# Kernel tuning notes

Measured on AMD Instinct MI355X. Metric: run time of the kernel, lower is better.

## Reference

```python
import jax, jax.numpy as jnp
import numpy as np

N, C, H, W = 128, 3, 256, 256
MAXNORM = 5.371920351148152
MAX_SQ = 16  # static bound for data-dependent squaring loop
PADE_B = [6.476475253248e+16, 3.238237626624e+16, 7771770303897600.0,
          1187353796428800.0, 129060195264000.0, 10559470521600.0,
          670442572800.0, 33522128640.0, 1323241920.0, 40840800.0,
          960960.0, 16380.0, 182.0, 1.0]


def pade13(A):
    b = PADE_B
    I = jnp.eye(A.shape[-1], dtype=A.dtype)
    A2 = A @ A
    A4 = A2 @ A2
    A6 = A4 @ A2
    U = A @ (A6 @ (b[13] * A6 + b[11] * A4 + b[9] * A2)
             + b[7] * A6 + b[5] * A4 + b[3] * A2 + b[1] * I)
    V = (A6 @ (b[12] * A6 + b[10] * A4 + b[8] * A2)
         + b[6] * A6 + b[4] * A4 + b[2] * A2 + b[0] * I)
    return U, V


def expm_affine(theta):  # theta: [N,2,3] -> exp of padded 3x3, top 2 rows
    n = theta.shape[0]
    A = jnp.concatenate([theta, jnp.zeros((n, 1, 3), theta.dtype)], axis=1)
    fro = jnp.sqrt(jnp.sum(A * A, axis=(1, 2), keepdims=True))
    n_sq = jnp.maximum(0.0, jnp.ceil(jnp.log2(fro / MAXNORM)))
    Asc = A / (2.0 ** n_sq)
    U, V = pade13(Asc)
    R = jnp.linalg.solve(U + V, -U + V)
    k = n_sq.reshape(n).astype(jnp.int32)
    def body(i, Rc):
        return jnp.where((i < k)[:, None, None], jnp.matmul(Rc, Rc), Rc)
    R = jax.lax.fori_loop(0, MAX_SQ, body, R)
    return R[:, :2, :]


def affine_grid(theta, Ho, Wo):  # align_corners=True
    xs = jnp.linspace(-1.0, 1.0, Wo, dtype=theta.dtype)
    ys = jnp.linspace(-1.0, 1.0, Ho, dtype=theta.dtype)
    gy, gx = jnp.meshgrid(ys, xs, indexing='ij')          # [Ho,Wo]
    base = jnp.stack([gx, gy, jnp.ones_like(gx)], axis=-1)  # [Ho,Wo,3]
    return jnp.einsum('hwk,nck->nhwc', base, theta)        # [N,Ho,Wo,2]


def grid_sample(x, grid):  # bilinear, zeros padding, align_corners=True
    _, _, Hi, Wi = x.shape
    ix = (grid[..., 0] + 1.0) * 0.5 * (Wi - 1)
    iy = (grid[..., 1] + 1.0) * 0.5 * (Hi - 1)
    ix0 = jnp.floor(ix)
    iy0 = jnp.floor(iy)
    ix1 = ix0 + 1.0
    iy1 = iy0 + 1.0
    wx1 = ix - ix0; wx0 = 1.0 - wx1
    wy1 = iy - iy0; wy0 = 1.0 - wy1

    def gather(yy, xx):
        valid = ((yy >= 0) & (yy < Hi) & (xx >= 0) & (xx < Wi))
        yc = jnp.clip(yy, 0, Hi - 1).astype(jnp.int32)
        xc = jnp.clip(xx, 0, Wi - 1).astype(jnp.int32)
        vals = jax.vmap(lambda img, y, xi: img[:, y, xi])(x, yc, xc)  # [N,C,Ho,Wo]
        return vals * valid[:, None].astype(x.dtype)

    return (gather(iy0, ix0) * (wy0 * wx0)[:, None]
            + gather(iy0, ix1) * (wy0 * wx1)[:, None]
            + gather(iy1, ix0) * (wy1 * wx0)[:, None]
            + gather(iy1, ix1) * (wy1 * wx1)[:, None])


def setup_inputs() -> dict:
    key = jax.random.key(0)
    k1, k2 = jax.random.split(key)
    x = jax.random.normal(k1, (N, C, H, W), dtype=jnp.float32)
    theta = 0.1 * jax.random.normal(k2, (N, 6), dtype=jnp.float32)
    return {"x": x, "theta": theta}


def reference(x, theta):
    th = expm_affine(theta.reshape(-1, 2, 3))  # [N,2,3]
    grid = affine_grid(th, H, W)               # [N,H,W,2]
    return grid_sample(x, grid)                # [N,C,H,W]
```

## Files before the change

### kernel.cpp

```cpp
#include <hip/hip_runtime.h>

#define Ndim 128
#define Cdim 3
#define Hdim 256
#define Wdim 256
#define HW (Hdim * Wdim)
#define MAXNORM_F 5.371920351148152f

typedef float vf2 __attribute__((ext_vector_type(2)));
typedef float vf4 __attribute__((ext_vector_type(4)));

__device__ __forceinline__ void mm3f(const float a[3][3], const float b[3][3], float c[3][3]) {
    #pragma unroll
    for (int i = 0; i < 3; ++i)
        #pragma unroll
        for (int j = 0; j < 3; ++j) {
            float s = 0.0f;
            #pragma unroll
            for (int k = 0; k < 3; ++k) s = fmaf(a[i][k], b[k][j], s);
            c[i][j] = s;
        }
}

__global__ void expm_kernel(const float* __restrict__ theta, float* __restrict__ thOut) {
    int n = blockIdx.x * blockDim.x + threadIdx.x;
    if (n >= Ndim) return;

    const float b[14] = {6.476475253248e+16f, 3.238237626624e+16f, 7771770303897600.0f,
                         1187353796428800.0f, 129060195264000.0f, 10559470521600.0f,
                         670442572800.0f, 33522128640.0f, 1323241920.0f, 40840800.0f,
                         960960.0f, 16380.0f, 182.0f, 1.0f};

    float A[3][3];
    #pragma unroll
    for (int j = 0; j < 3; ++j) {
        A[0][j] = theta[n * 6 + j];
        A[1][j] = theta[n * 6 + 3 + j];
        A[2][j] = 0.0f;
    }

    float fro2 = 0.0f;
    #pragma unroll
    for (int i = 0; i < 3; ++i)
        #pragma unroll
        for (int j = 0; j < 3; ++j) fro2 = fmaf(A[i][j], A[i][j], fro2);
    float fro = sqrtf(fro2);

    float nsq = fmaxf(0.0f, ceilf(log2f(fro / MAXNORM_F)));
    int k = (int)nsq;
    float sc = exp2f(-nsq);
    #pragma unroll
    for (int i = 0; i < 3; ++i)
        #pragma unroll
        for (int j = 0; j < 3; ++j) A[i][j] *= sc;

    float A2[3][3], A4[3][3], A6[3][3], P[3][3], Wm[3][3], T[3][3], U[3][3], V[3][3];
    mm3f(A, A, A2);
    mm3f(A2, A2, A4);
    mm3f(A4, A2, A6);

    #pragma unroll
    for (int i = 0; i < 3; ++i)
        #pragma unroll
        for (int j = 0; j < 3; ++j)
            P[i][j] = b[13] * A6[i][j] + b[11] * A4[i][j] + b[9] * A2[i][j];
    mm3f(A6, P, T);
    #pragma unroll
    for (int i = 0; i < 3; ++i)
        #pragma unroll
        for (int j = 0; j < 3; ++j)
            Wm[i][j] = T[i][j] + b[7] * A6[i][j] + b[5] * A4[i][j] + b[3] * A2[i][j]
                       + (i == j ? b[1] : 0.0f);
    mm3f(A, Wm, U);

    #pragma unroll
    for (int i = 0; i < 3; ++i)
        #pragma unroll
        for (int j = 0; j < 3; ++j)
            P[i][j] = b[12] * A6[i][j] + b[10] * A4[i][j] + b[8] * A2[i][j];
    mm3f(A6, P, T);
    #pragma unroll
    for (int i = 0; i < 3; ++i)
        #pragma unroll
        for (int j = 0; j < 3; ++j)
            V[i][j] = T[i][j] + b[6] * A6[i][j] + b[4] * A4[i][j] + b[2] * A2[i][j]
                      + (i == j ? b[0] : 0.0f);

    float M[3][6];
    #pragma unroll
    for (int i = 0; i < 3; ++i)
        #pragma unroll
        for (int j = 0; j < 3; ++j) {
            M[i][j]     = U[i][j] + V[i][j];
            M[i][j + 3] = V[i][j] - U[i][j];
        }
    #pragma unroll
    for (int col = 0; col < 3; ++col) {
        int piv = col;
        float best = fabsf(M[col][col]);
        for (int r = col + 1; r < 3; ++r) {
            float v = fabsf(M[r][col]);
            if (v > best) { best = v; piv = r; }
        }
        if (piv != col) {
            #pragma unroll
            for (int j = 0; j < 6; ++j) {
                float t = M[col][j]; M[col][j] = M[piv][j]; M[piv][j] = t;
            }
        }
        float inv = 1.0f / M[col][col];
        #pragma unroll
        for (int j = 0; j < 6; ++j) M[col][j] *= inv;
        #pragma unroll
        for (int r = 0; r < 3; ++r) {
            if (r == col) continue;
            float f = M[r][col];
            #pragma unroll
            for (int j = 0; j < 6; ++j) M[r][j] -= f * M[col][j];
        }
    }
    float R[3][3];
    #pragma unroll
    for (int i = 0; i < 3; ++i)
        #pragma unroll
        for (int j = 0; j < 3; ++j) R[i][j] = M[i][j + 3];

    for (int i = 0; i < 16; ++i) {
        if (i < k) {
            float Rn[3][3];
            mm3f(R, R, Rn);
            #pragma unroll
            for (int a = 0; a < 3; ++a)
                #pragma unroll
                for (int c = 0; c < 3; ++c) R[a][c] = Rn[a][c];
        }
    }

    #pragma unroll
    for (int j = 0; j < 3; ++j) {
        thOut[n * 6 + j]     = (float)R[0][j];
        thOut[n * 6 + 3 + j] = (float)R[1][j];
    }
}

__global__ __launch_bounds__(256) void sample_kernel(const float* __restrict__ x,
                                                     const float* __restrict__ th,
                                                     float* __restrict__ out) {
    const int nwg_per_xcd = 8192 / 8;
    int bid = blockIdx.x;
    int wgid = (bid & 7) * nwg_per_xcd + (bid >> 3);

    int tw  = wgid & 3;
    int thp = (wgid >> 2) & 15;
    int n   = wgid >> 6;

    int tid = threadIdx.x;
    int wp  = tid & 31;
    int hp  = tid >> 5;
    int w0  = (tw << 6) + (wp << 1);
    int h0  = (thp << 4) + (hp << 1);

    const float* t = th + n * 6;
    float t0 = t[0], t1 = t[1], t2 = t[2], t3 = t[3], t4 = t[4], t5 = t[5];

    float Cx = 127.5f * (t2 - t0 - t1 + 1.0f);
    float Cy = 127.5f * (t5 - t3 - t4 + 1.0f);

    float ix00 = fmaf((float)w0, t0, fmaf((float)h0, t1, Cx));
    float iy00 = fmaf((float)w0, t3, fmaf((float)h0, t4, Cy));
    float ix[2][2] = {{ix00, ix00 + t0}, {ix00 + t1, ix00 + t0 + t1}};
    float iy[2][2] = {{iy00, iy00 + t3}, {iy00 + t4, iy00 + t3 + t4}};

    size_t nbase = (size_t)n * Cdim * HW;
    bool fast = (fabsf(t0) + fabsf(t1) < 2.0f) && (fabsf(t3) + fabsf(t4) < 2.0f);

    if (fast) {
        float Xminf = fminf(fminf(ix[0][0], ix[0][1]), fminf(ix[1][0], ix[1][1]));
        float Yminf = fminf(fminf(iy[0][0], iy[0][1]), fminf(iy[1][0], iy[1][1]));
        int Xmin = (int)floorf(Xminf);
        int Ymin = (int)floorf(Yminf);
        int bx = min(max(Xmin, 0), Wdim - 4);

        float wxv[2][2][4], wyv[2][2][4];
        #pragma unroll
        for (int p = 0; p < 2; ++p)
            #pragma unroll
            for (int q = 0; q < 2; ++q) {
                float fx = floorf(ix[p][q]);
                float fy = floorf(iy[p][q]);
                int ixi = (int)fx, iyi = (int)fy;
                float wx1 = ix[p][q] - fx, wx0 = 1.0f - wx1;
                float wy1 = iy[p][q] - fy, wy0 = 1.0f - wy1;
                float mx0 = ((unsigned)ixi       < (unsigned)Wdim) ? 1.0f : 0.0f;
                float mx1 = ((unsigned)(ixi + 1) < (unsigned)Wdim) ? 1.0f : 0.0f;
                float my0 = ((unsigned)iyi       < (unsigned)Hdim) ? 1.0f : 0.0f;
                float my1 = ((unsigned)(iyi + 1) < (unsigned)Hdim) ? 1.0f : 0.0f;
                float wxm0 = wx0 * mx0, wxm1 = wx1 * mx1;
                float wym0 = wy0 * my0, wym1 = wy1 * my1;

                int cxa = min(max(ixi, 0), Wdim - 1) - bx;
                int cxb = min(max(ixi + 1, 0), Wdim - 1) - bx;
                int rya = iyi - Ymin;
                #pragma unroll
                for (int j = 0; j < 4; ++j) {
                    wxv[p][q][j] = (j == cxa ? wxm0 : 0.0f) + (j == cxb ? wxm1 : 0.0f);
                    wyv[p][q][j] = (j == rya ? wym0 : 0.0f) + (j == rya + 1 ? wym1 : 0.0f);
                }
            }

        int roff[4];
        #pragma unroll
        for (int i = 0; i < 4; ++i) {
            int r = min(max(Ymin + i, 0), Hdim - 1);
            roff[i] = (r << 8) + bx;
        }

        const float* img0 = x + nbase;
        const float* img1 = img0 + HW;
        const float* img2 = img1 + HW;
        vf4 R0[4], R1[4], R2[4];
        #pragma unroll
        for (int i = 0; i < 4; ++i) __builtin_memcpy(&R0[i], img0 + roff[i], 16);
        #pragma unroll
        for (int i = 0; i < 4; ++i) __builtin_memcpy(&R1[i], img1 + roff[i], 16);
        #pragma unroll
        for (int i = 0; i < 4; ++i) __builtin_memcpy(&R2[i], img2 + roff[i], 16);

        size_t p0 = (size_t)h0 * Wdim + w0;
        size_t p1 = p0 + Wdim;

        #pragma unroll
        for (int c = 0; c < Cdim; ++c) {
            const vf4* Rw = (c == 0) ? R0 : (c == 1) ? R1 : R2;
            float res[2][2];
            #pragma unroll
            for (int p = 0; p < 2; ++p)
                #pragma unroll
                for (int q = 0; q < 2; ++q) {
                    float s = 0.0f;
                    #pragma unroll
                    for (int i = 0; i < 4; ++i) {
                        vf4 rv = Rw[i];
                        float d = fmaf(rv.x, wxv[p][q][0],
                                  fmaf(rv.y, wxv[p][q][1],
                                  fmaf(rv.z, wxv[p][q][2],
                                       rv.w * wxv[p][q][3])));
                        s = fmaf(wyv[p][q][i], d, s);
                    }
                    res[p][q] = s;
                }
            vf2 r0 = {res[0][0], res[0][1]};
            vf2 r1 = {res[1][0], res[1][1]};
            __builtin_nontemporal_store(r0, (vf2*)(out + nbase + (size_t)c * HW + p0));
            __builtin_nontemporal_store(r1, (vf2*)(out + nbase + (size_t)c * HW + p1));
        }
    } else {
        const float* img0 = x + nbase;
        #pragma unroll
        for (int p = 0; p < 2; ++p)
            #pragma unroll
            for (int q = 0; q < 2; ++q) {
                float fx = floorf(ix[p][q]);
                float fy = floorf(iy[p][q]);
                int ix0 = (int)fx, iy0 = (int)fy;
                float wx1 = ix[p][q] - fx, wx0 = 1.0f - wx1;
                float wy1 = iy[p][q] - fy, wy0 = 1.0f - wy1;
                float mx0 = ((unsigned)ix0       < (unsigned)Wdim) ? 1.0f : 0.0f;
                float mx1 = ((unsigned)(ix0 + 1) < (unsigned)Wdim) ? 1.0f : 0.0f;
                float my0 = ((unsigned)iy0       < (unsigned)Hdim) ? 1.0f : 0.0f;
                float my1 = ((unsigned)(iy0 + 1) < (unsigned)Hdim) ? 1.0f : 0.0f;
                int xc0 = min(max(ix0, 0), Wdim - 1);
                int xc1 = min(max(ix0 + 1, 0), Wdim - 1);
                int yc0 = min(max(iy0, 0), Hdim - 1);
                int yc1 = min(max(iy0 + 1, 0), Hdim - 1);
                float w00 = wy0 * wx0 * my0 * mx0;
                float w01 = wy0 * wx1 * my0 * mx1;
                float w10 = wy1 * wx0 * my1 * mx0;
                float w11 = wy1 * wx1 * my1 * mx1;
                int o00 = yc0 * Wdim + xc0, o01 = yc0 * Wdim + xc1;
                int o10 = yc1 * Wdim + xc0, o11 = yc1 * Wdim + xc1;
                #pragma unroll
                for (int c = 0; c < Cdim; ++c) {
                    const float* img = img0 + (size_t)c * HW;
                    float r = fmaf(img[o00], w00, fmaf(img[o01], w01,
                              fmaf(img[o10], w10, img[o11] * w11)));
                    out[nbase + (size_t)c * HW + (size_t)(h0 + p) * Wdim + (w0 + q)] = r;
                }
            }
    }
}

extern "C" void kernel_launch(void* const* d_in, const int* in_sizes, int n_in,
                              void* d_out, int out_size, void* d_ws, size_t ws_size,
                              hipStream_t stream) {
    const float* x     = (const float*)d_in[0];
    const float* theta = (const float*)d_in[1];
    float* out = (float*)d_out;
    float* th  = (float*)d_ws;

    expm_kernel<<<1, 128, 0, stream>>>(theta, th);

    int nblocks = Ndim * 16 * 4;
    sample_kernel<<<nblocks, 256, 0, stream>>>(x, th, out);
}
```

Baseline: 42.27 us.

## Stage bounding-box source patch in LDS via global_load_lds with square tiles

Each workgroup now covers a 32x32 output tile instead of 16x64. It computes the bounding box of the source pixels that tile needs and loads that patch for all three channels into shared memory with direct global-to-LDS loads. Each thread then does its bilinear taps from LDS instead of issuing per-thread 4x4 vector global loads, which cuts redundant global and L2 traffic. The cost is a barrier and about 40KB of LDS per workgroup, which may lower occupancy. Tiles whose patch exceeds the LDS buffer fall back to the direct-gather path.

```diff
diff --git a/kernel.cpp b/kernel.cpp
--- a/kernel.cpp
+++ b/kernel.cpp
@@ -8,7 +8,7 @@
 #define MAXNORM_F 5.371920351148152f
 
 typedef float vf2 __attribute__((ext_vector_type(2)));
-typedef float vf4 __attribute__((ext_vector_type(4)));
+typedef unsigned int uint32;
 
 __device__ __forceinline__ void mm3f(const float a[3][3], const float b[3][3], float c[3][3]) {
     #pragma unroll
@@ -146,19 +146,20 @@
 __global__ __launch_bounds__(256) void sample_kernel(const float* __restrict__ x,
                                                      const float* __restrict__ th,
                                                      float* __restrict__ out) {
+    __shared__ float lds[10240];
+
     const int nwg_per_xcd = 8192 / 8;
     int bid = blockIdx.x;
     int wgid = (bid & 7) * nwg_per_xcd + (bid >> 3);
 
-    int tw  = wgid & 3;
-    int thp = (wgid >> 2) & 15;
+    int tw  = wgid & 7;
+    int thp = (wgid >> 3) & 7;
     int n   = wgid >> 6;
 
     int tid = threadIdx.x;
-    int wp  = tid & 31;
-    int hp  = tid >> 5;
-    int w0  = (tw << 6) + (wp << 1);
-    int h0  = (thp << 4) + (hp << 1);
+    int wp = tid & 15, hp = tid >> 4;
+    int w0 = (tw << 5) + (wp << 1);
+    int h0 = (thp << 5) + (hp << 1);
 
     const float* t = th + n * 6;
     float t0 = t[0], t1 = t[1], t2 = t[2], t3 = t[3], t4 = t[4], t5 = t[5];
@@ -166,93 +167,90 @@
     float Cx = 127.5f * (t2 - t0 - t1 + 1.0f);
     float Cy = 127.5f * (t5 - t3 - t4 + 1.0f);
 
+    float fwA = (float)(tw << 5),  fwB = fwA + 31.0f;
+    float fhA = (float)(thp << 5), fhB = fhA + 31.0f;
+    float xlo = fminf(fwA * t0, fwB * t0) + fminf(fhA * t1, fhB * t1) + Cx;
+    float xhi = fmaxf(fwA * t0, fwB * t0) + fmaxf(fhA * t1, fhB * t1) + Cx;
+    float ylo = fminf(fwA * t3, fwB * t3) + fminf(fhA * t4, fhB * t4) + Cy;
+    float yhi = fmaxf(fwA * t3, fwB * t3) + fmaxf(fhA * t4, fhB * t4) + Cy;
+    int Xlo = (int)floorf(xlo) - 1, Xhi = (int)floorf(xhi) + 2;
+    int Ylo = (int)floorf(ylo) - 1, Yhi = (int)floorf(yhi) + 2;
+    int cn = Xhi - Xlo + 1;
+    int rn = Yhi - Ylo + 1;
+
+    size_t nbase = (size_t)n * Cdim * HW;
+
     float ix00 = fmaf((float)w0, t0, fmaf((float)h0, t1, Cx));
     float iy00 = fmaf((float)w0, t3, fmaf((float)h0, t4, Cy));
-    float ix[2][2] = {{ix00, ix00 + t0}, {ix00 + t1, ix00 + t0 + t1}};
-    float iy[2][2] = {{iy00, iy00 + t3}, {iy00 + t4, iy00 + t3 + t4}};
-
-    size_t nbase = (size_t)n * Cdim * HW;
-    bool fast = (fabsf(t0) + fabsf(t1) < 2.0f) && (fabsf(t3) + fabsf(t4) < 2.0f);
+    float ixq[2][2] = {{ix00, ix00 + t0}, {ix00 + t1, ix00 + t0 + t1}};
+    float iyq[2][2] = {{iy00, iy00 + t3}, {iy00 + t4, iy00 + t3 + t4}};
+
+    bool fast = (cn <= 52) && (rn <= 55) && (rn >= 1) && (cn >= 1);
 
     if (fast) {
-        float Xminf = fminf(fminf(ix[0][0], ix[0][1]), fminf(ix[1][0], ix[1][1]));
-        float Yminf = fminf(fminf(iy[0][0], iy[0][1]), fminf(iy[1][0], iy[1][1]));
-        int Xmin = (int)floorf(Xminf);
-        int Ymin = (int)floorf(Yminf);
-        int bx = min(max(Xmin, 0), Wdim - 4);
-
-        float wxv[2][2][4], wyv[2][2][4];
+        int bxw = (min(max(Xlo, 0), Wdim - 56)) & ~3;
+        int byw = min(max(Ylo, 0), Hdim - rn);
+
+        int totc  = 42 * (rn + 1);
+        int iters = (totc + 255) >> 8;
+        const float* gbase = x + nbase;
+        for (int it = 0; it < iters; ++it) {
+            int c = (it << 8) + tid;
+            int row = c / 42;
+            int rem = c - row * 42;
+            row = min(row, rn);
+            int ch   = rem / 14;
+            int colc = rem - ch * 14;
+            int srow = min(byw + row, Hdim - 1);
+            const float* gp = gbase + (size_t)ch * HW + (srow << 8) + bxw + (colc << 2);
+            __builtin_amdgcn_global_load_lds(
+                (const __attribute__((address_space(1))) uint32*)gp,
+                (__attribute__((address_space(3))) uint32*)((uint32*)lds + ((size_t)c << 2)),
+                16, 0, 0);
+        }
+        __syncthreads();
+
+        float res[2][2][3];
         #pragma unroll
         for (int p = 0; p < 2; ++p)
             #pragma unroll
             for (int q = 0; q < 2; ++q) {
-                float fx = floorf(ix[p][q]);
-                float fy = floorf(iy[p][q]);
-                int ixi = (int)fx, iyi = (int)fy;
-                float wx1 = ix[p][q] - fx, wx0 = 1.0f - wx1;
-                float wy1 = iy[p][q] - fy, wy0 = 1.0f - wy1;
-                float mx0 = ((unsigned)ixi       < (unsigned)Wdim) ? 1.0f : 0.0f;
-                float mx1 = ((unsigned)(ixi + 1) < (unsigned)Wdim) ? 1.0f : 0.0f;
-                float my0 = ((unsigned)iyi       < (unsigned)Hdim) ? 1.0f : 0.0f;
-                float my1 = ((unsigned)(iyi + 1) < (unsigned)Hdim) ? 1.0f : 0.0f;
+                float ix = ixq[p][q], iy = iyq[p][q];
+                float fx = floorf(ix), fy = floorf(iy);
+                int x0i = (int)fx, y0i = (int)fy;
+                float wx1 = ix - fx, wx0 = 1.0f - wx1;
+                float wy1 = iy - fy, wy0 = 1.0f - wy1;
+                float mx0 = ((unsigned)x0i       < (unsigned)Wdim) ? 1.0f : 0.0f;
+                float mx1 = ((unsigned)(x0i + 1) < (unsigned)Wdim) ? 1.0f : 0.0f;
+                float my0 = ((unsigned)y0i       < (unsigned)Hdim) ? 1.0f : 0.0f;
+                float my1 = ((unsigned)(y0i + 1) < (unsigned)Hdim) ? 1.0f : 0.0f;
                 float wxm0 = wx0 * mx0, wxm1 = wx1 * mx1;
                 float wym0 = wy0 * my0, wym1 = wy1 * my1;
 
-                int cxa = min(max(ixi, 0), Wdim - 1) - bx;
-                int cxb = min(max(ixi + 1, 0), Wdim - 1) - bx;
-                int rya = iyi - Ymin;
+                int lx0 = min(max(x0i - bxw, 0), 55);
+                int lx1 = min(max(x0i + 1 - bxw, 0), 55);
+                int ly0 = min(max(y0i - byw, 0), rn);
+                int ly1 = min(max(y0i + 1 - byw, 0), rn);
+                int r0 = ly0 * 168, r1 = ly1 * 168;
                 #pragma unroll
-                for (int j = 0; j < 4; ++j) {
-                    wxv[p][q][j] = (j == cxa ? wxm0 : 0.0f) + (j == cxb ? wxm1 : 0.0f);
-                    wyv[p][q][j] = (j == rya ? wym0 : 0.0f) + (j == rya + 1 ? wym1 : 0.0f);
+                for (int c = 0; c < Cdim; ++c) {
+                    int b0 = r0 + c * 56;
+                    int b1 = r1 + c * 56;
+                    float v00 = lds[b0 + lx0], v01 = lds[b0 + lx1];
+                    float v10 = lds[b1 + lx0], v11 = lds[b1 + lx1];
+                    float top = fmaf(v01, wxm1, v00 * wxm0);
+                    float bot = fmaf(v11, wxm1, v10 * wxm0);
+                    res[p][q][c] = fmaf(wym1, bot, wym0 * top);
                 }
             }
 
-        int roff[4];
-        #pragma unroll
-        for (int i = 0; i < 4; ++i) {
-            int r = min(max(Ymin + i, 0), Hdim - 1);
-            roff[i] = (r << 8) + bx;
-        }
-
-        const float* img0 = x + nbase;
-        const float* img1 = img0 + HW;
-        const float* img2 = img1 + HW;
-        vf4 R0[4], R1[4], R2[4];
-        #pragma unroll
-        for (int i = 0; i < 4; ++i) __builtin_memcpy(&R0[i], img0 + roff[i], 16);
-        #pragma unroll
-        for (int i = 0; i < 4; ++i) __builtin_memcpy(&R1[i], img1 + roff[i], 16);
-        #pragma unroll
-        for (int i = 0; i < 4; ++i) __builtin_memcpy(&R2[i], img2 + roff[i], 16);
-
         size_t p0 = (size_t)h0 * Wdim + w0;
-        size_t p1 = p0 + Wdim;
-
         #pragma unroll
         for (int c = 0; c < Cdim; ++c) {
-            const vf4* Rw = (c == 0) ? R0 : (c == 1) ? R1 : R2;
-            float res[2][2];
-            #pragma unroll
-            for (int p = 0; p < 2; ++p)
-                #pragma unroll
-                for (int q = 0; q < 2; ++q) {
-                    float s = 0.0f;
-                    #pragma unroll
-                    for (int i = 0; i < 4; ++i) {
-                        vf4 rv = Rw[i];
-                        float d = fmaf(rv.x, wxv[p][q][0],
-                                  fmaf(rv.y, wxv[p][q][1],
-                                  fmaf(rv.z, wxv[p][q][2],
-                                       rv.w * wxv[p][q][3])));
-                        s = fmaf(wyv[p][q][i], d, s);
-                    }
-                    res[p][q] = s;
-                }
-            vf2 r0 = {res[0][0], res[0][1]};
-            vf2 r1 = {res[1][0], res[1][1]};
+            vf2 r0 = {res[0][0][c], res[0][1][c]};
+            vf2 r1 = {res[1][0][c], res[1][1][c]};
             __builtin_nontemporal_store(r0, (vf2*)(out + nbase + (size_t)c * HW + p0));
-            __builtin_nontemporal_store(r1, (vf2*)(out + nbase + (size_t)c * HW + p1));
+            __builtin_nontemporal_store(r1, (vf2*)(out + nbase + (size_t)c * HW + p0 + Wdim));
         }
     } else {
         const float* img0 = x + nbase;
@@ -260,11 +258,11 @@
         for (int p = 0; p < 2; ++p)
             #pragma unroll
             for (int q = 0; q < 2; ++q) {
-                float fx = floorf(ix[p][q]);
-                float fy = floorf(iy[p][q]);
+                float ix = ixq[p][q], iy = iyq[p][q];
+                float fx = floorf(ix), fy = floorf(iy);
                 int ix0 = (int)fx, iy0 = (int)fy;
-                float wx1 = ix[p][q] - fx, wx0 = 1.0f - wx1;
-                float wy1 = iy[p][q] - fy, wy0 = 1.0f - wy1;
+                float wx1 = ix - fx, wx0 = 1.0f - wx1;
+                float wy1 = iy - fy, wy0 = 1.0f - wy1;
                 float mx0 = ((unsigned)ix0       < (unsigned)Wdim) ? 1.0f : 0.0f;
                 float mx1 = ((unsigned)(ix0 + 1) < (unsigned)Wdim) ? 1.0f : 0.0f;
                 float my0 = ((unsigned)iy0       < (unsigned)Hdim) ? 1.0f : 0.0f;
@@ -300,6 +298,6 @@
 
     expm_kernel<<<1, 128, 0, stream>>>(theta, th);
 
-    int nblocks = Ndim * 16 * 4;
+    int nblocks = 8192;
     sample_kernel<<<nblocks, 256, 0, stream>>>(x, th, out);
 }
```

After: 43.32 us. 2.5% more time.
